# Kernel tuning notes

Measured on AMD Instinct MI355X. Metric: run time of the kernel, lower is better.

The kernel has to match this reference:

```python
import jax, jax.numpy as jnp
import numpy as np

V, E, H, T, B, A = 100000, 300, 256, 128, 64, 8
FH, NC = 256, 2
G = 2 * H  # gcn_input_dim = hidden_size * 2


def setup_inputs() -> dict:
    key = jax.random.key(0)
    ks = jax.random.split(key, 28)
    def n(k, shape, scale=0.05):
        return jax.random.normal(k, shape, dtype=jnp.float32) * scale
    return {
        "sentence": jax.random.randint(ks[0], (B, T), 0, V),
        "aspect": jax.random.randint(ks[1], (B, A), 0, V),
        "pos_class": jax.random.randint(ks[2], (B, T), 0, 18),
        "dep_tags": jax.random.randint(ks[3], (B, T), 0, 40),
        "text_len": jax.random.randint(ks[4], (B,), 1, T + 1),
        "aspect_len": jax.random.randint(ks[5], (B,), 1, A + 1),
        "dep_rels": jax.random.randint(ks[6], (B, T), 0, 40),
        "dep_heads": jax.random.randint(ks[7], (B, T), 0, T),
        "aspect_position": jax.random.randint(ks[8], (B, T), 0, 2),
        "dep_dirs": jax.random.randint(ks[9], (B, T), 0, 3),
        # frozen GloVe table
        "glove_emb": jax.random.normal(ks[10], (V, E), dtype=jnp.float32),
        # BiLSTM (1 layer): PyTorch layout, gates ordered i,f,g,o
        "w_ih_f": n(ks[11], (4 * H, E)), "w_hh_f": n(ks[12], (4 * H, H)),
        "b_ih_f": n(ks[13], (4 * H,)), "b_hh_f": n(ks[14], (4 * H,)),
        "w_ih_b": n(ks[15], (4 * H, E)), "w_hh_b": n(ks[16], (4 * H, H)),
        "b_ih_b": n(ks[17], (4 * H,)), "b_hh_b": n(ks[18], (4 * H,)),
        # 'gcn' attention branch: self.gat = nn.Linear(G, G)
        "gat_w": n(ks[19], (G, G)), "gat_b": n(ks[20], (G,)),
        # fcs MLP (num_mlps = 2)
        "fc1_w": n(ks[21], (FH, G)), "fc1_b": n(ks[22], (FH,)),
        "fc2_w": n(ks[23], (FH, FH)), "fc2_b": n(ks[24], (FH,)),
        "fcf_w": n(ks[25], (NC, FH)), "fcf_b": n(ks[26], (NC,)),
    }


def _lstm_dir(x, w_ih, w_hh, b_ih, b_hh, reverse):
    """One direction of a PyTorch-style LSTM. x: (B, T, E) -> (B, T, H)."""
    Bn = x.shape[0]
    Hh = w_hh.shape[1]
    xs = jnp.swapaxes(x, 0, 1)  # (T, B, E)
    if reverse:
        xs = xs[::-1]
    def step(carry, xt):
        h, c = carry
        g = xt @ w_ih.T + b_ih + h @ w_hh.T + b_hh  # (B, 4H)
        i, f, gg, o = jnp.split(g, 4, axis=-1)
        c = jax.nn.sigmoid(f) * c + jax.nn.sigmoid(i) * jnp.tanh(gg)
        h = jax.nn.sigmoid(o) * jnp.tanh(c)
        return (h, c), h
    init = (jnp.zeros((Bn, Hh), x.dtype), jnp.zeros((Bn, Hh), x.dtype))
    _, hs = jax.lax.scan(step, init, xs)
    if reverse:
        hs = hs[::-1]
    return jnp.swapaxes(hs, 0, 1)


def _bilstm(x, w_ih_f, w_hh_f, b_ih_f, b_hh_f, w_ih_b, w_hh_b, b_ih_b, b_hh_b):
    fwd = _lstm_dir(x, w_ih_f, w_hh_f, b_ih_f, b_hh_f, reverse=False)
    bwd = _lstm_dir(x, w_ih_b, w_hh_b, b_ih_b, b_hh_b, reverse=True)
    return jnp.concatenate([fwd, bwd], axis=-1)  # (B, T, 2H)


def reference(sentence, aspect, pos_class, dep_tags, text_len, aspect_len,
              dep_rels, dep_heads, aspect_position, dep_dirs,
              glove_emb, w_ih_f, w_hh_f, b_ih_f, b_hh_f,
              w_ih_b, w_hh_b, b_ih_b, b_hh_b,
              gat_w, gat_b, fc1_w, fc1_b, fc2_w, fc2_b, fcf_w, fcf_b):
    # fmask: per-token validity mask derived from text_len (inputs_to_deprel_adj)
    fmask = (jnp.arange(T)[None, :] < text_len[:, None]).astype(jnp.float32)  # (B, T)
    # embedding lookup (dropout is identity in eval mode)
    feature = glove_emb[sentence]  # (B, T, E)
    # BiLSTM over the sentence. (aspect branch is dead code in the 'gcn' path:
    # aspect_feature is computed but never used, so we omit it.)
    feature = _bilstm(feature, w_ih_f, w_hh_f, b_ih_f, b_hh_f,
                      w_ih_b, w_hh_b, b_ih_b, b_hh_b)  # (B, T, 2H)
    # 'gcn' branch: linear, mask, sum over tokens, relu
    gat_out = feature @ gat_w.T + gat_b           # (B, T, 2H)
    gat_out = gat_out * fmask[:, :, None]
    gat_out = jax.nn.relu(jnp.sum(gat_out, axis=1))  # (B, 2H)
    # fcs MLP + final classifier
    x = jax.nn.relu(gat_out @ fc1_w.T + fc1_b)
    x = jax.nn.relu(x @ fc2_w.T + fc2_b)
    logit = x @ fcf_w.T + fcf_b                    # (B, NC)
    return logit
```

## Files before the change

### kernel.cpp

```cpp
#include <hip/hip_runtime.h>
#include <hip/hip_bf16.h>
#include <math.h>

#define B_  64
#define T_  128
#define E_  300
#define H_  256
#define G4  1024
#define N2  2048
#define GG  512
#define FH_ 256
#define NC_ 2
#define KP  320

typedef __attribute__((ext_vector_type(8))) short short8;
typedef __attribute__((ext_vector_type(4))) float f32x4;
typedef unsigned short ushort_t;
typedef unsigned long long u64;

static __device__ __forceinline__ ushort_t bf16bits(float x) {
    __hip_bfloat16 b = __float2bfloat16(x);
    return __builtin_bit_cast(ushort_t, b);
}
static __device__ __forceinline__ float bf16lo(unsigned v) {
    return __builtin_bit_cast(float, v << 16);
}
static __device__ __forceinline__ float bf16hi(unsigned v) {
    return __builtin_bit_cast(float, v & 0xffff0000u);
}

#define OFF_BIAS  262144
#define OFF_WIH   524288
#define OFF_XEMB  2097152
#define OFF_XPROJ 8388608
#define OFF_S     41943040

__global__ __launch_bounds__(256) void k_prep(
    const int*   __restrict__ sentence,
    const float* __restrict__ glove,
    const float* __restrict__ w_ih_f,
    const float* __restrict__ w_ih_b,
    const float* __restrict__ b_ih_f, const float* __restrict__ b_hh_f,
    const float* __restrict__ b_ih_b, const float* __restrict__ b_hh_b,
    u64*         __restrict__ hbuf,
    float*       __restrict__ bias2,
    ushort_t*    __restrict__ wihshuf,
    ushort_t*    __restrict__ xemb) {
    const int idx = blockIdx.x * 256 + threadIdx.x;

    if (idx < 16384) hbuf[idx] = 0ull;

    if (idx < N2) {
        bias2[idx] = (idx < G4) ? (b_ih_f[idx] + b_hh_f[idx])
                                : (b_ih_b[idx - G4] + b_hh_b[idx - G4]);
    }

    if (idx < 81920) {
        const int ntile = idx / 640;
        const int r     = idx % 640;
        const int ks    = r / 64;
        const int lane  = r % 64;
        const int n  = ntile * 16 + (lane & 15);
        const int k0 = ks * 32 + ((lane >> 4) << 3);
        const float* src = (n < G4) ? (w_ih_f + (size_t)n * E_)
                                    : (w_ih_b + (size_t)(n - G4) * E_);
        ushort_t o[8];
        #pragma unroll
        for (int j = 0; j < 8; ++j) {
            const int k = k0 + j;
            o[j] = (k < E_) ? bf16bits(src[k]) : (ushort_t)0;
        }
        uint4 pk;
        pk.x = (unsigned)o[0] | ((unsigned)o[1] << 16);
        pk.y = (unsigned)o[2] | ((unsigned)o[3] << 16);
        pk.z = (unsigned)o[4] | ((unsigned)o[5] << 16);
        pk.w = (unsigned)o[6] | ((unsigned)o[7] << 16);
        *(uint4*)(wihshuf + (size_t)idx * 8) = pk;
    }

    {
        const int m  = idx / 80;
        const int c4 = (idx % 80) * 4;
        const float* row = glove + (size_t)sentence[m] * E_;
        ushort_t o[4];
        #pragma unroll
        for (int j = 0; j < 4; ++j) {
            const int k = c4 + j;
            o[j] = (k < E_) ? bf16bits(row[k]) : (ushort_t)0;
        }
        uint2 pk;
        pk.x = (unsigned)o[0] | ((unsigned)o[1] << 16);
        pk.y = (unsigned)o[2] | ((unsigned)o[3] << 16);
        *(uint2*)(xemb + (size_t)m * KP + c4) = pk;
    }
}

__global__ __launch_bounds__(256) void k_xproj_mfma(
    const ushort_t* __restrict__ xemb,
    const ushort_t* __restrict__ wihshuf,
    const float*    __restrict__ bias2,
    ushort_t*       __restrict__ xprojb) {
    __shared__ ushort_t ct[4][16][136];
    const int tid = threadIdx.x;
    const int wave = tid >> 6, lane = tid & 63;
    const int quad = lane >> 4, l15 = lane & 15;
    const int m0 = blockIdx.x * 64 + wave * 16;
    const ushort_t* ap = xemb + (size_t)(m0 + l15) * KP;
    const ushort_t* wp = wihshuf + (size_t)blockIdx.y * 40960 + lane * 8;

    f32x4 acc[8] = {};
    #pragma unroll
    for (int ks = 0; ks < 10; ++ks) {
        short8 af = *(const short8*)(ap + ks * 32 + quad * 8);
        #pragma unroll
        for (int j = 0; j < 8; ++j) {
            short8 bf = *(const short8*)(wp + (size_t)(j * 10 + ks) * 512);
            acc[j] = __builtin_amdgcn_mfma_f32_16x16x32_bf16(af, bf, acc[j], 0, 0, 0);
        }
    }
    #pragma unroll
    for (int j = 0; j < 8; ++j) {
        const float bias = bias2[blockIdx.y * 128 + j * 16 + l15];
        #pragma unroll
        for (int r = 0; r < 4; ++r)
            ct[wave][quad * 4 + r][j * 16 + l15] = bf16bits(acc[j][r] + bias);
    }
    #pragma unroll
    for (int i = 0; i < 4; ++i) {
        const int row = i * 4 + (lane >> 4);
        uint4 v = *(const uint4*)&ct[wave][row][l15 * 8];
        *(uint4*)(xprojb + (size_t)(m0 + row) * N2 + blockIdx.y * 128 + l15 * 8) = v;
    }
}

__global__ __launch_bounds__(256, 1) void k_lstm_sync(
    const ushort_t* __restrict__ xprojb,
    const float*    __restrict__ w_hh_f,
    const float*    __restrict__ w_hh_b,
    const int*      __restrict__ text_len,
    u64*            __restrict__ hbuf,
    float*          __restrict__ S)
{
    __shared__ ushort_t hl[16][264];
    __shared__ float    gLDS[4 * 16 * 33];

    const int tid   = threadIdx.x;
    const int g     = blockIdx.x & 7;
    const int slice = blockIdx.x >> 3;
    const int d     = g & 1;
    const int b0    = (g >> 1) * 16;
    const int j0    = slice * 32;
    const int wave  = tid >> 6, lane = tid & 63;
    const int quad  = lane >> 4, l15 = lane & 15;

    const float* whh = d ? w_hh_b : w_hh_f;
    u64* slab0 = hbuf + (size_t)g * 2048;
    u64* slab1 = hbuf + 16384 + (size_t)g * 2048;

    short8 wfrag[2][8];
    #pragma unroll
    for (int u = 0; u < 2; ++u) {
        const int n = wave * 256 + j0 + u * 16 + l15;
        #pragma unroll
        for (int ks = 0; ks < 8; ++ks) {
            const float* p = whh + (size_t)n * 256 + ks * 32 + quad * 8;
            float4 lo = *(const float4*)p;
            float4 hi = *(const float4*)(p + 4);
            short8 f;
            f[0] = (short)bf16bits(lo.x); f[1] = (short)bf16bits(lo.y);
            f[2] = (short)bf16bits(lo.z); f[3] = (short)bf16bits(lo.w);
            f[4] = (short)bf16bits(hi.x); f[5] = (short)bf16bits(hi.y);
            f[6] = (short)bf16bits(hi.z); f[7] = (short)bf16bits(hi.w);
            wfrag[u][ks] = f;
        }
    }

    const int mb = tid >> 4;
    const int wi = mb * 128 + slice * 16 + (tid & 15);
    const int c0 = (tid & 15) * 2;
    const int lenm = text_len[b0 + mb];
    float cst0 = 0.f, cst1 = 0.f, s0 = 0.f, s1 = 0.f;

    for (int t = 0; t < T_; ++t) {
        const int tt = d ? (T_ - 1 - t) : t;
        const ushort_t* xp = xprojb +
            ((size_t)(b0 + mb) * T_ + tt) * N2 + d * G4 + j0;
        const unsigned vi = *(const unsigned*)(xp + c0);
        const unsigned vf = *(const unsigned*)(xp + 256 + c0);
        const unsigned vg = *(const unsigned*)(xp + 512 + c0);
        const unsigned vo = *(const unsigned*)(xp + 768 + c0);

        if (wave == 0) {
            const u64* src = ((t & 1) ? slab1 : slab0) +
                             (lane & 15) * 128 + (lane >> 4) * 32;
            u64 v[32];
            bool ok = false;
            while (!ok) {
                ok = true;
                #pragma unroll
                for (int i = 0; i < 32; ++i)
                    v[i] = __hip_atomic_load(src + i, __ATOMIC_RELAXED,
                                             __HIP_MEMORY_SCOPE_AGENT);
                #pragma unroll
                for (int i = 0; i < 32; ++i)
                    ok = ok && ((unsigned)(v[i] >> 32) == (unsigned)t);
            }
            ushort_t* drow = &hl[lane & 15][(lane >> 4) * 64];
            #pragma unroll
            for (int i = 0; i < 16; ++i) {
                uint2 pk;
                pk.x = (unsigned)v[2 * i];
                pk.y = (unsigned)v[2 * i + 1];
                *(uint2*)(drow + i * 4) = pk;
            }
        }
        __syncthreads();

        short8 af[8];
        #pragma unroll
        for (int ks = 0; ks < 8; ++ks)
            af[ks] = *(const short8*)&hl[l15][ks * 32 + quad * 8];
        f32x4 acc[2] = {};
        #pragma unroll
        for (int ks = 0; ks < 8; ++ks) {
            acc[0] = __builtin_amdgcn_mfma_f32_16x16x32_bf16(
                af[ks], wfrag[0][ks], acc[0], 0, 0, 0);
            acc[1] = __builtin_amdgcn_mfma_f32_16x16x32_bf16(
                af[ks], wfrag[1][ks], acc[1], 0, 0, 0);
        }
        #pragma unroll
        for (int u = 0; u < 2; ++u)
            #pragma unroll
            for (int r = 0; r < 4; ++r)
                gLDS[wave * 528 + (quad * 4 + r) * 33 + u * 16 + l15] = acc[u][r];
        __syncthreads();

        const int gb = mb * 33 + c0;
        const float gi0 = gLDS[gb],        gi1 = gLDS[gb + 1];
        const float gf0 = gLDS[528 + gb],  gf1 = gLDS[528 + gb + 1];
        const float gg0 = gLDS[1056 + gb], gg1 = gLDS[1056 + gb + 1];
        const float go0 = gLDS[1584 + gb], go1 = gLDS[1584 + gb + 1];
        const float i0 = 1.f / (1.f + __expf(-(bf16lo(vi) + gi0)));
        const float i1 = 1.f / (1.f + __expf(-(bf16hi(vi) + gi1)));
        const float f0 = 1.f / (1.f + __expf(-(bf16lo(vf) + gf0)));
        const float f1 = 1.f / (1.f + __expf(-(bf16hi(vf) + gf1)));
        const float gc0 = tanhf(bf16lo(vg) + gg0);
        const float gc1 = tanhf(bf16hi(vg) + gg1);
        const float o0 = 1.f / (1.f + __expf(-(bf16lo(vo) + go0)));
        const float o1 = 1.f / (1.f + __expf(-(bf16hi(vo) + go1)));
        cst0 = f0 * cst0 + i0 * gc0;
        cst1 = f1 * cst1 + i1 * gc1;
        const float h0 = o0 * tanhf(cst0);
        const float h1 = o1 * tanhf(cst1);
        if (tt < lenm) { s0 += h0; s1 += h1; }

        const u64 word = ((u64)(unsigned)(t + 1) << 32) |
                         (u64)((unsigned)bf16bits(h0) |
                               ((unsigned)bf16bits(h1) << 16));
        u64* dst = ((t & 1) ? slab0 : slab1) + wi;
        __hip_atomic_store(dst, word, __ATOMIC_RELAXED,
                           __HIP_MEMORY_SCOPE_AGENT);
    }

    float2 sv; sv.x = s0; sv.y = s1;
    *(float2*)(S + (size_t)(b0 + mb) * GG + d * H_ + j0 + c0) = sv;
}

__global__ __launch_bounds__(256) void k_head(
    const float* __restrict__ S,
    const int*   __restrict__ text_len,
    const float* __restrict__ gat_w, const float* __restrict__ gat_b,
    const float* __restrict__ fc1_w, const float* __restrict__ fc1_b,
    const float* __restrict__ fc2_w, const float* __restrict__ fc2_b,
    const float* __restrict__ fcf_w, const float* __restrict__ fcf_b,
    float* __restrict__ out)
{
    __shared__ float sb[GG];
    __shared__ float x1[GG];
    __shared__ float x2[FH_];
    __shared__ float x3[FH_];
    const int b = blockIdx.x, tid = threadIdx.x;
    sb[tid]       = S[(size_t)b * GG + tid];
    sb[tid + 256] = S[(size_t)b * GG + tid + 256];
    __syncthreads();
    const float lenf = (float)text_len[b];
    #pragma unroll
    for (int r = 0; r < 2; ++r) {
        const int n = tid + r * 256;
        float acc = gat_b[n] * lenf;
        const float* w = gat_w + (size_t)n * GG;
        for (int k = 0; k < GG; ++k) acc += sb[k] * w[k];
        x1[n] = fmaxf(acc, 0.f);
    }
    __syncthreads();
    {
        float acc = fc1_b[tid];
        const float* w = fc1_w + (size_t)tid * GG;
        for (int k = 0; k < GG; ++k) acc += x1[k] * w[k];
        x2[tid] = fmaxf(acc, 0.f);
    }
    __syncthreads();
    {
        float acc = fc2_b[tid];
        const float* w = fc2_w + (size_t)tid * FH_;
        for (int k = 0; k < FH_; ++k) acc += x2[k] * w[k];
        x3[tid] = fmaxf(acc, 0.f);
    }
    __syncthreads();
    if (tid < NC_) {
        float acc = fcf_b[tid];
        const float* w = fcf_w + (size_t)tid * FH_;
        for (int k = 0; k < FH_; ++k) acc += x3[k] * w[k];
        out[b * NC_ + tid] = acc;
    }
}

extern "C" void kernel_launch(void* const* d_in, const int* in_sizes, int n_in,
                              void* d_out, int out_size, void* d_ws, size_t ws_size,
                              hipStream_t stream) {
    const int*   sentence = (const int*)  d_in[0];
    const int*   text_len = (const int*)  d_in[4];
    const float* glove    = (const float*)d_in[10];
    const float* w_ih_f   = (const float*)d_in[11];
    const float* w_hh_f   = (const float*)d_in[12];
    const float* b_ih_f   = (const float*)d_in[13];
    const float* b_hh_f   = (const float*)d_in[14];
    const float* w_ih_b   = (const float*)d_in[15];
    const float* w_hh_b   = (const float*)d_in[16];
    const float* b_ih_b   = (const float*)d_in[17];
    const float* b_hh_b   = (const float*)d_in[18];
    const float* gat_w    = (const float*)d_in[19];
    const float* gat_b    = (const float*)d_in[20];
    const float* fc1_w    = (const float*)d_in[21];
    const float* fc1_b    = (const float*)d_in[22];
    const float* fc2_w    = (const float*)d_in[23];
    const float* fc2_b    = (const float*)d_in[24];
    const float* fcf_w    = (const float*)d_in[25];
    const float* fcf_b    = (const float*)d_in[26];
    float* out = (float*)d_out;

    char* ws = (char*)d_ws;
    u64*      hbuf    = (u64*)ws;
    float*    bias2   = (float*)(ws + OFF_BIAS);
    ushort_t* wihshuf = (ushort_t*)(ws + OFF_WIH);
    ushort_t* xemb    = (ushort_t*)(ws + OFF_XEMB);
    ushort_t* xprojb  = (ushort_t*)(ws + OFF_XPROJ);
    float*    S       = (float*)(ws + OFF_S);

    k_prep<<<2560, 256, 0, stream>>>(sentence, glove, w_ih_f, w_ih_b,
                                     b_ih_f, b_hh_f, b_ih_b, b_hh_b,
                                     hbuf, bias2, wihshuf, xemb);
    dim3 gx(128, 16);
    k_xproj_mfma<<<gx, 256, 0, stream>>>(xemb, wihshuf, bias2, xprojb);
    k_lstm_sync<<<64, 256, 0, stream>>>(xprojb, w_hh_f, w_hh_b, text_len,
                                        hbuf, S);
    k_head<<<64, 256, 0, stream>>>(S, text_len, gat_w, gat_b,
                                   fc1_w, fc1_b, fc2_w, fc2_b,
                                   fcf_w, fcf_b, out);
}
```

Measured before the change: 746.8 us.

## Spread h-exchange polling across all waves with sc0 fast path and atomic fallback

The per-step hidden-state exchange between blocks now has every thread poll its own 8 words instead of wave 0 polling 32 words each. A second mirrored buffer is read with inline-asm sc0 loads for a bounded number of tries, then falls back to agent-scope atomic loads on the original buffer. The aim is lower latency on the serial per-step barrier. Sigmoid and tanh also switch to fast-divide exp formulas. The cost is two stores per step, a more complex protocol that relies on cache-coherence behaviour, and slightly lower accuracy in the activations.

```diff
diff --git a/kernel.cpp b/kernel.cpp
--- a/kernel.cpp
+++ b/kernel.cpp
@@ -29,8 +29,36 @@
     return __builtin_bit_cast(float, v & 0xffff0000u);
 }
 
+static __device__ __forceinline__ float sigm_f(float x) {
+    return __fdividef(1.f, 1.f + __expf(-x));
+}
+static __device__ __forceinline__ float tanh_f(float x) {
+    return 1.f - __fdividef(2.f, __expf(2.f * x) + 1.f);
+}
+
+static __device__ __forceinline__ void ld8_sc0(const u64* p, u64 v[8]) {
+    u64 r0, r1, r2, r3, r4, r5, r6, r7;
+    asm volatile(
+        "global_load_dwordx2 %0, %8, off sc0\n\t"
+        "global_load_dwordx2 %1, %8, off offset:8 sc0\n\t"
+        "global_load_dwordx2 %2, %8, off offset:16 sc0\n\t"
+        "global_load_dwordx2 %3, %8, off offset:24 sc0\n\t"
+        "global_load_dwordx2 %4, %8, off offset:32 sc0\n\t"
+        "global_load_dwordx2 %5, %8, off offset:40 sc0\n\t"
+        "global_load_dwordx2 %6, %8, off offset:48 sc0\n\t"
+        "global_load_dwordx2 %7, %8, off offset:56 sc0\n\t"
+        "s_waitcnt vmcnt(0)"
+        : "=&v"(r0), "=&v"(r1), "=&v"(r2), "=&v"(r3),
+          "=&v"(r4), "=&v"(r5), "=&v"(r6), "=&v"(r7)
+        : "v"(p)
+        : "memory");
+    v[0] = r0; v[1] = r1; v[2] = r2; v[3] = r3;
+    v[4] = r4; v[5] = r5; v[6] = r6; v[7] = r7;
+}
+
 #define OFF_BIAS  262144
 #define OFF_WIH   524288
+#define OFF_A     1835008
 #define OFF_XEMB  2097152
 #define OFF_XPROJ 8388608
 #define OFF_S     41943040
@@ -42,13 +70,14 @@
     const float* __restrict__ w_ih_b,
     const float* __restrict__ b_ih_f, const float* __restrict__ b_hh_f,
     const float* __restrict__ b_ih_b, const float* __restrict__ b_hh_b,
-    u64*         __restrict__ hbuf,
+    u64*         __restrict__ hbufB,
+    u64*         __restrict__ hbufA,
     float*       __restrict__ bias2,
     ushort_t*    __restrict__ wihshuf,
     ushort_t*    __restrict__ xemb) {
     const int idx = blockIdx.x * 256 + threadIdx.x;
 
-    if (idx < 16384) hbuf[idx] = 0ull;
+    if (idx < 16384) { hbufB[idx] = 0ull; hbufA[idx] = 0ull; }
 
     if (idx < N2) {
         bias2[idx] = (idx < G4) ? (b_ih_f[idx] + b_hh_f[idx])
@@ -138,7 +167,8 @@
     const float*    __restrict__ w_hh_f,
     const float*    __restrict__ w_hh_b,
     const int*      __restrict__ text_len,
-    u64*            __restrict__ hbuf,
+    u64*            __restrict__ hbufB,
+    u64*            __restrict__ hbufA,
     float*          __restrict__ S)
 {
     __shared__ ushort_t hl[16][264];
@@ -154,8 +184,10 @@
     const int quad  = lane >> 4, l15 = lane & 15;
 
     const float* whh = d ? w_hh_b : w_hh_f;
-    u64* slab0 = hbuf + (size_t)g * 2048;
-    u64* slab1 = hbuf + 16384 + (size_t)g * 2048;
+    u64* slabB0 = hbufB + (size_t)g * 2048;
+    u64* slabB1 = hbufB + 16384 + (size_t)g * 2048;
+    u64* slabA0 = hbufA + (size_t)g * 2048;
+    u64* slabA1 = hbufA + 16384 + (size_t)g * 2048;
 
     short8 wfrag[2][8];
     #pragma unroll
@@ -175,11 +207,13 @@
         }
     }
 
-    const int mb = tid >> 4;
-    const int wi = mb * 128 + slice * 16 + (tid & 15);
-    const int c0 = (tid & 15) * 2;
+    const int mb  = tid >> 4;
+    const int pp0 = (tid & 15) * 8;
+    const int wi  = mb * 128 + slice * 16 + (tid & 15);
+    const int c0  = (tid & 15) * 2;
     const int lenm = text_len[b0 + mb];
     float cst0 = 0.f, cst1 = 0.f, s0 = 0.f, s1 = 0.f;
+    bool slow = false;
 
     for (int t = 0; t < T_; ++t) {
         const int tt = d ? (T_ - 1 - t) : t;
@@ -190,29 +224,42 @@
         const unsigned vg = *(const unsigned*)(xp + 512 + c0);
         const unsigned vo = *(const unsigned*)(xp + 768 + c0);
 
-        if (wave == 0) {
-            const u64* src = ((t & 1) ? slab1 : slab0) +
-                             (lane & 15) * 128 + (lane >> 4) * 32;
-            u64 v[32];
-            bool ok = false;
-            while (!ok) {
-                ok = true;
+        const u64* srcA = ((t & 1) ? slabA1 : slabA0) + mb * 128 + pp0;
+        const u64* srcB = ((t & 1) ? slabB1 : slabB0) + mb * 128 + pp0;
+        u64 v[8];
+        bool need = true;
+        if (!slow) {
+            for (int tries = 0; tries < 48 && need; ++tries) {
+                ld8_sc0(srcA, v);
+                bool ok = true;
                 #pragma unroll
-                for (int i = 0; i < 32; ++i)
-                    v[i] = __hip_atomic_load(src + i, __ATOMIC_RELAXED,
+                for (int i = 0; i < 8; ++i)
+                    ok = ok && ((unsigned)(v[i] >> 32) == (unsigned)t);
+                if (ok) need = false;
+            }
+            if (need) slow = true;
+        }
+        if (need) {
+            for (;;) {
+                #pragma unroll
+                for (int i = 0; i < 8; ++i)
+                    v[i] = __hip_atomic_load(srcB + i, __ATOMIC_RELAXED,
                                              __HIP_MEMORY_SCOPE_AGENT);
+                bool ok = true;
                 #pragma unroll
-                for (int i = 0; i < 32; ++i)
+                for (int i = 0; i < 8; ++i)
                     ok = ok && ((unsigned)(v[i] >> 32) == (unsigned)t);
+                if (ok) break;
             }
-            ushort_t* drow = &hl[lane & 15][(lane >> 4) * 64];
-            #pragma unroll
-            for (int i = 0; i < 16; ++i) {
-                uint2 pk;
-                pk.x = (unsigned)v[2 * i];
-                pk.y = (unsigned)v[2 * i + 1];
-                *(uint2*)(drow + i * 4) = pk;
-            }
+        }
+        {
+            uint4 pk0, pk1;
+            pk0.x = (unsigned)v[0]; pk0.y = (unsigned)v[1];
+            pk0.z = (unsigned)v[2]; pk0.w = (unsigned)v[3];
+            pk1.x = (unsigned)v[4]; pk1.y = (unsigned)v[5];
+            pk1.z = (unsigned)v[6]; pk1.w = (unsigned)v[7];
+            *(uint4*)&hl[mb][pp0 * 2]     = pk0;
+            *(uint4*)&hl[mb][pp0 * 2 + 8] = pk1;
         }
         __syncthreads();
 
@@ -240,25 +287,27 @@
         const float gf0 = gLDS[528 + gb],  gf1 = gLDS[528 + gb + 1];
         const float gg0 = gLDS[1056 + gb], gg1 = gLDS[1056 + gb + 1];
         const float go0 = gLDS[1584 + gb], go1 = gLDS[1584 + gb + 1];
-        const float i0 = 1.f / (1.f + __expf(-(bf16lo(vi) + gi0)));
-        const float i1 = 1.f / (1.f + __expf(-(bf16hi(vi) + gi1)));
-        const float f0 = 1.f / (1.f + __expf(-(bf16lo(vf) + gf0)));
-        const float f1 = 1.f / (1.f + __expf(-(bf16hi(vf) + gf1)));
-        const float gc0 = tanhf(bf16lo(vg) + gg0);
-        const float gc1 = tanhf(bf16hi(vg) + gg1);
-        const float o0 = 1.f / (1.f + __expf(-(bf16lo(vo) + go0)));
-        const float o1 = 1.f / (1.f + __expf(-(bf16hi(vo) + go1)));
+        const float i0 = sigm_f(bf16lo(vi) + gi0);
+        const float i1 = sigm_f(bf16hi(vi) + gi1);
+        const float f0 = sigm_f(bf16lo(vf) + gf0);
+        const float f1 = sigm_f(bf16hi(vf) + gf1);
+        const float gc0 = tanh_f(bf16lo(vg) + gg0);
+        const float gc1 = tanh_f(bf16hi(vg) + gg1);
+        const float o0 = sigm_f(bf16lo(vo) + go0);
+        const float o1 = sigm_f(bf16hi(vo) + go1);
         cst0 = f0 * cst0 + i0 * gc0;
         cst1 = f1 * cst1 + i1 * gc1;
-        const float h0 = o0 * tanhf(cst0);
-        const float h1 = o1 * tanhf(cst1);
+        const float h0 = o0 * tanh_f(cst0);
+        const float h1 = o1 * tanh_f(cst1);
         if (tt < lenm) { s0 += h0; s1 += h1; }
 
         const u64 word = ((u64)(unsigned)(t + 1) << 32) |
                          (u64)((unsigned)bf16bits(h0) |
                                ((unsigned)bf16bits(h1) << 16));
-        u64* dst = ((t & 1) ? slab0 : slab1) + wi;
-        __hip_atomic_store(dst, word, __ATOMIC_RELAXED,
+        u64* dstA = ((t & 1) ? slabA0 : slabA1) + wi;
+        u64* dstB = ((t & 1) ? slabB0 : slabB1) + wi;
+        *(volatile u64*)dstA = word;
+        __hip_atomic_store(dstB, word, __ATOMIC_RELAXED,
                            __HIP_MEMORY_SCOPE_AGENT);
     }
 
@@ -340,20 +389,21 @@
     float* out = (float*)d_out;
 
     char* ws = (char*)d_ws;
-    u64*      hbuf    = (u64*)ws;
+    u64*      hbufB   = (u64*)ws;
     float*    bias2   = (float*)(ws + OFF_BIAS);
     ushort_t* wihshuf = (ushort_t*)(ws + OFF_WIH);
+    u64*      hbufA   = (u64*)(ws + OFF_A);
     ushort_t* xemb    = (ushort_t*)(ws + OFF_XEMB);
     ushort_t* xprojb  = (ushort_t*)(ws + OFF_XPROJ);
     float*    S       = (float*)(ws + OFF_S);
 
     k_prep<<<2560, 256, 0, stream>>>(sentence, glove, w_ih_f, w_ih_b,
                                      b_ih_f, b_hh_f, b_ih_b, b_hh_b,
-                                     hbuf, bias2, wihshuf, xemb);
+                                     hbufB, hbufA, bias2, wihshuf, xemb);
     dim3 gx(128, 16);
     k_xproj_mfma<<<gx, 256, 0, stream>>>(xemb, wihshuf, bias2, xprojb);
     k_lstm_sync<<<64, 256, 0, stream>>>(xprojb, w_hh_f, w_hh_b, text_len,
-                                        hbuf, S);
+                                        hbufB, hbufA, S);
     k_head<<<64, 256, 0, stream>>>(S, text_len, gat_w, gat_b,
                                    fc1_w, fc1_b, fc2_w, fc2_b,
                                    fcf_w, fcf_b, out);
```

New measurement: 711.4 us. 4.7% less time.
